# Kernel tuning notes

Hardware: AMD Instinct MI355X
Metric: run time of the kernel (lower is better)

The kernel has to match this reference:

```python
import jax, jax.numpy as jnp
import numpy as np

B, S, C, D = 2, 2048, 2048, 128
H = C // D
EPS = 1.1920928955078125e-07  # torch finfo(float32).eps (RMSNorm default eps=None)


def rms_norm(x, g):
    # x: [..., D], normalized over last dim, elementwise affine g
    var = jnp.mean(jnp.square(x), axis=-1, keepdims=True)
    return x * jax.lax.rsqrt(var + EPS) * g


def apply_rotary(x, rope):
    # x: [B,S,H,D]; rope: [S,1,D/2,2,2] (2x2 rotation matrices)
    b, s, h, d = x.shape
    x_ = x.reshape(b, s, h, d // 2, 1, 2)
    out = jnp.sum(rope * x_, axis=-1)  # [B,S,H,D/2,2]
    return out.reshape(b, s, h, d)


def setup_inputs() -> dict:
    key = jax.random.key(0)
    ks = jax.random.split(key, 10)
    sc = 1.0 / np.sqrt(C)
    return {
        "x": jax.random.normal(ks[0], (B, S, C), jnp.float32),
        "rope": jax.random.normal(ks[1], (S, 1, D // 2, 2, 2), jnp.float32),
        "Wq": jax.random.normal(ks[2], (C, C), jnp.float32) * sc,
        "bq": jnp.zeros((C,), jnp.float32),
        "Wk": jax.random.normal(ks[3], (C, C), jnp.float32) * sc,
        "bk": jnp.zeros((C,), jnp.float32),
        "Wv": jax.random.normal(ks[4], (C, C), jnp.float32) * sc,
        "bv": jnp.zeros((C,), jnp.float32),
        "gq": jnp.ones((D,), jnp.float32),
        "gk": jnp.ones((D,), jnp.float32),
        "Wo": jax.random.normal(ks[5], (C, C), jnp.float32) * sc,
        "bo": jnp.zeros((C,), jnp.float32),
    }


def reference(x, rope, Wq, bq, Wk, bk, Wv, bv, gq, gk, Wo, bo):
    b, s, _ = x.shape
    # QKV projections (torch Linear: x @ W.T + b)
    q = (x @ Wq.T + bq).reshape(b, s, H, D)
    k = (x @ Wk.T + bk).reshape(b, s, H, D)
    v = (x @ Wv.T + bv).reshape(b, s, H, D)
    # per-head RMSNorm on q/k (computed in fp32 as in the original)
    q = rms_norm(q, gq)
    k = rms_norm(k, gk)
    # rotary embedding via 2x2 rotation matrices
    q = apply_rotary(q, rope)
    k = apply_rotary(k, rope)
    # scaled dot-product attention (non-causal)
    scale = 1.0 / jnp.sqrt(jnp.asarray(D, q.dtype))
    scores = jnp.einsum("bqhd,bkhd->bhqk", q, k) * scale
    attn = jax.nn.softmax(scores, axis=-1)
    out = jnp.einsum("bhqk,bkhd->bqhd", attn, v).reshape(b, s, C)
    return out @ Wo.T + bo
```

## Files before the change

kernel.cpp:

```cpp
#include <hip/hip_runtime.h>
#include <hip/hip_bf16.h>


typedef __bf16 bf16_t;
typedef __bf16 bf16x2 __attribute__((ext_vector_type(2)));
typedef __bf16 bf16x4 __attribute__((ext_vector_type(4)));
typedef __bf16 bf16x8 __attribute__((ext_vector_type(8)));
typedef float  f32x4  __attribute__((ext_vector_type(4)));

#define EPSF 1.1920928955078125e-07f
#define QSCALE 0.1275310039f

__device__ __forceinline__ void load_lds16(const void* g, void* l) {
  __builtin_amdgcn_global_load_lds((__attribute__((address_space(1))) void*)(g),
                                   (__attribute__((address_space(3))) void*)(l),
                                   16, 0, 0);
}

__global__ __launch_bounds__(256) void castk(const float4* __restrict__ src,
                                             bf16x4* __restrict__ dst, int n4) {
  int i = blockIdx.x * blockDim.x + threadIdx.x;
  int stride = gridDim.x * blockDim.x;
  for (; i < n4; i += stride) {
    float4 v = src[i];
    bf16x4 o;
    o.x = (bf16_t)v.x; o.y = (bf16_t)v.y; o.z = (bf16_t)v.z; o.w = (bf16_t)v.w;
    dst[i] = o;
  }
}

template <int MODE>
__global__ __launch_bounds__(256, 2)
void gemm_bt(const bf16_t* __restrict__ A, const bf16_t* __restrict__ B,
             int M, int N, int K,
             const float* __restrict__ bias0, const float* __restrict__ bias1,
             const float* __restrict__ bias2,
             float* __restrict__ outf,
             bf16_t* __restrict__ qb, bf16_t* __restrict__ kb, bf16_t* __restrict__ vb) {
  __shared__ bf16_t As[128 * 64];
  __shared__ bf16_t Bs[128 * 64];
  const int t = threadIdx.x, l = t & 63, w = t >> 6;
  const int lq = l & 15, grp = l >> 4;

  int flat = blockIdx.y * gridDim.x + blockIdx.x;
  int nwg = gridDim.x * gridDim.y;
  int cpx = nwg >> 3;
  int wg = (flat & 7) * cpx + (flat >> 3);
  int bx = wg % gridDim.x, by = wg / gridDim.x;
  const int bRow = by * 128, bCol = bx * 128;
  const int wr = w >> 1, wc = w & 1;

  const int srow = w * 8 + (l >> 3);
  const int scol = ((l & 7) ^ (l >> 3)) * 8;
  const bf16_t* Ag = A + (size_t)(bRow + srow) * K + scol;
  const bf16_t* Bg = B + (size_t)(bCol + srow) * K + scol;
  const int dstbase = w * 1024;

  f32x4 acc[4][4];
  const f32x4 zf = {0.f, 0.f, 0.f, 0.f};
#pragma unroll
  for (int i = 0; i < 4; ++i)
#pragma unroll
    for (int j = 0; j < 4; ++j) acc[i][j] = zf;

  const int arow = wr * 64 + lq;
  const int brow = wc * 64 + lq;
  const int axor = l & 7;

  for (int k0 = 0; k0 < K; k0 += 64) {
#pragma unroll
    for (int c = 0; c < 4; ++c)
      load_lds16(Ag + (size_t)c * 32 * K, (char*)As + c * 4096 + dstbase);
#pragma unroll
    for (int c = 0; c < 4; ++c)
      load_lds16(Bg + (size_t)c * 32 * K, (char*)Bs + c * 4096 + dstbase);
    Ag += 64; Bg += 64;
    __syncthreads();
#pragma unroll
    for (int kk = 0; kk < 2; ++kk) {
      bf16x8 af[4], bfv[4];
#pragma unroll
      for (int i = 0; i < 4; ++i)
        af[i] = *(const bf16x8*)((const char*)As + (arow + i * 16) * 128 +
                                 (((kk << 2) + grp) ^ axor) * 16);
#pragma unroll
      for (int j = 0; j < 4; ++j)
        bfv[j] = *(const bf16x8*)((const char*)Bs + (brow + j * 16) * 128 +
                                  (((kk << 2) + grp) ^ axor) * 16);
#pragma unroll
      for (int i = 0; i < 4; ++i)
#pragma unroll
        for (int j = 0; j < 4; ++j)
          acc[i][j] = __builtin_amdgcn_mfma_f32_16x16x32_bf16(af[i], bfv[j], acc[i][j], 0, 0, 0);
    }
    __syncthreads();
  }

  if (MODE == 0) {
    const int part = bCol >> 11;
    const int hd_base = bCol & 2047;
    const int h = hd_base >> 7;
    const float* bias = part == 0 ? bias0 : part == 1 ? bias1 : bias2;
    bf16_t* dst = part == 0 ? qb : part == 1 ? kb : vb;
#pragma unroll
    for (int i = 0; i < 4; ++i)
#pragma unroll
      for (int j = 0; j < 4; ++j)
#pragma unroll
        for (int r = 0; r < 4; ++r) {
          int m = bRow + wr * 64 + i * 16 + grp * 4 + r;
          int d = wc * 64 + j * 16 + lq;
          int bb = m >> 11, s = m & 2047;
          float v = acc[i][j][r] + bias[hd_base + d];
          dst[(((size_t)bb * 16 + h) * 2048 + s) * 128 + d] = (bf16_t)v;
        }
  } else {
#pragma unroll
    for (int i = 0; i < 4; ++i)
#pragma unroll
      for (int j = 0; j < 4; ++j)
#pragma unroll
        for (int r = 0; r < 4; ++r) {
          int m = bRow + wr * 64 + i * 16 + grp * 4 + r;
          int n = bCol + wc * 64 + j * 16 + lq;
          outf[(size_t)m * N + n] = acc[i][j][r] + bias0[n];
        }
  }
}

__global__ __launch_bounds__(256)
void normrope(bf16_t* __restrict__ q, bf16_t* __restrict__ k,
              const float* __restrict__ rope,
              const float* __restrict__ gq, const float* __restrict__ gk) {
  const int l = threadIdx.x & 63, wv = threadIdx.x >> 6;
  const int rid = blockIdx.x * 4 + wv;
  const int s = rid & 2047;
  const size_t base = (size_t)rid * 128 + 2 * l;
  const float4 rp = *(const float4*)(rope + ((size_t)s * 64 + l) * 4);
  const float g0q = gq[2 * l], g1q = gq[2 * l + 1];
  const float g0k = gk[2 * l], g1k = gk[2 * l + 1];

  {
    bf16x2 xq = *(const bf16x2*)(q + base);
    float x0 = (float)xq.x, x1 = (float)xq.y;
    float ss = x0 * x0 + x1 * x1;
#pragma unroll
    for (int off = 1; off < 64; off <<= 1) ss += __shfl_xor(ss, off);
    float rs = rsqrtf(ss * (1.f / 128.f) + EPSF);
    float n0 = x0 * rs * g0q, n1 = x1 * rs * g1q;
    bf16x2 o;
    o.x = (bf16_t)((rp.x * n0 + rp.y * n1) * QSCALE);
    o.y = (bf16_t)((rp.z * n0 + rp.w * n1) * QSCALE);
    *(bf16x2*)(q + base) = o;
  }
  {
    bf16x2 xk = *(const bf16x2*)(k + base);
    float x0 = (float)xk.x, x1 = (float)xk.y;
    float ss = x0 * x0 + x1 * x1;
#pragma unroll
    for (int off = 1; off < 64; off <<= 1) ss += __shfl_xor(ss, off);
    float rs = rsqrtf(ss * (1.f / 128.f) + EPSF);
    float n0 = x0 * rs * g0k, n1 = x1 * rs * g1k;
    bf16x2 o;
    o.x = (bf16_t)(rp.x * n0 + rp.y * n1);
    o.y = (bf16_t)(rp.z * n0 + rp.w * n1);
    *(bf16x2*)(k + base) = o;
  }
}

__global__ __launch_bounds__(256)
void transpose_v(const bf16_t* __restrict__ v, bf16_t* __restrict__ vt) {
  __shared__ bf16_t st[64][68];
  const int t = threadIdx.x;
  const int bh = blockIdx.z;
  const int s0 = blockIdx.x * 64, d0 = blockIdx.y * 64;
  const bf16_t* vp = v + (size_t)bh * 2048 * 128;
  bf16_t* vtp = vt + (size_t)bh * 128 * 2048;
  const int r = t >> 4, c = (t & 15) * 4;
#pragma unroll
  for (int p = 0; p < 4; ++p) {
    bf16x4 x = *(const bf16x4*)(vp + (size_t)(s0 + r + p * 16) * 128 + d0 + c);
    *(bf16x4*)&st[r + p * 16][c] = x;
  }
  __syncthreads();
#pragma unroll
  for (int p = 0; p < 4; ++p) {
    int dr = r + p * 16;
    bf16x4 y;
    y.x = st[c + 0][dr]; y.y = st[c + 1][dr]; y.z = st[c + 2][dr]; y.w = st[c + 3][dr];
    *(bf16x4*)(vtp + (size_t)(d0 + dr) * 2048 + s0 + c) = y;
  }
}

__global__ __launch_bounds__(256, 2)
void attn_fwd(const bf16_t* __restrict__ Q, const bf16_t* __restrict__ K,
              const bf16_t* __restrict__ VT, bf16_t* __restrict__ O) {
  __shared__ char smem[81920];
  const int t = threadIdx.x, l = t & 63, wv = t >> 6;
  const int lq = l & 15, grp = l >> 4;
  const int bid = blockIdx.x;
  const int xcd = bid & 7, ksid = bid >> 3;
  const int bh = ((ksid >> 4) << 3) | xcd;
  const int qbi = ksid & 15;
  const int b_ = bh >> 4, h = bh & 15;
  const bf16_t* Qp = Q + (size_t)bh * 2048 * 128;
  const bf16_t* Kp = K + (size_t)bh * 2048 * 128;
  const bf16_t* Vp = VT + (size_t)bh * 128 * 2048;
  const int q0 = qbi * 128 + wv * 32;
  const int axor = lq & 7;

  int ksoff[4], vsoff[4], dstoff[4];
#pragma unroll
  for (int i = 0; i < 4; ++i) {
    int g = (i * 4 + wv) * 64 + l;
    int kr = g >> 4, kc = g & 15;
    ksoff[i] = kr * 256 + ((kc ^ (kr & 7)) << 4);
    int vr = g >> 3, vc = g & 7;
    vsoff[i] = vr * 4096 + ((vc ^ (vr & 7)) << 4);
    dstoff[i] = (i * 4 + wv) * 1024;
  }

  bf16x8 qf[2][4];
#pragma unroll
  for (int qt = 0; qt < 2; ++qt)
#pragma unroll
    for (int c = 0; c < 4; ++c)
      qf[qt][c] = *(const bf16x8*)(Qp + (size_t)(q0 + qt * 16 + lq) * 128 + c * 32 + grp * 8);

  f32x4 o[2][8];
  const f32x4 zf = {0.f, 0.f, 0.f, 0.f};
#pragma unroll
  for (int a = 0; a < 2; ++a)
#pragma unroll
    for (int d = 0; d < 8; ++d) o[a][d] = zf;
  float m_run[2] = {-1e30f, -1e30f}, l_run[2] = {0.f, 0.f};
  char* pb = smem + 65536 + wv * 4096;

  auto stage = [&](int buf, int kvb) {
    char* kdst = smem + buf * 16384;
    char* vdst = smem + 32768 + buf * 16384;
    const char* ksrc = (const char*)Kp + (size_t)kvb * 256;
    const char* vsrc = (const char*)Vp + (size_t)kvb * 2;
#pragma unroll
    for (int i = 0; i < 4; ++i) load_lds16(ksrc + ksoff[i], kdst + dstoff[i]);
#pragma unroll
    for (int i = 0; i < 4; ++i) load_lds16(vsrc + vsoff[i], vdst + dstoff[i]);
  };

  stage(0, 0);
  __syncthreads();

  for (int it = 0; it < 32; ++it) {
    const int cur = it & 1;
    if (it < 31) stage(cur ^ 1, (it + 1) * 64);
    const char* kb = smem + cur * 16384;
    const char* vb = smem + 32768 + cur * 16384;

    f32x4 sc[4][2];
#pragma unroll
    for (int kvt = 0; kvt < 4; ++kvt) { sc[kvt][0] = zf; sc[kvt][1] = zf; }
    __builtin_amdgcn_s_setprio(1);
#pragma unroll
    for (int kvt = 0; kvt < 4; ++kvt)
#pragma unroll
      for (int c = 0; c < 4; ++c) {
        bf16x8 kf = *(const bf16x8*)(kb + (kvt * 16 + lq) * 256 +
                                     ((((c << 2) + grp) ^ axor) << 4));
        sc[kvt][0] = __builtin_amdgcn_mfma_f32_16x16x32_bf16(kf, qf[0][c], sc[kvt][0], 0, 0, 0);
        sc[kvt][1] = __builtin_amdgcn_mfma_f32_16x16x32_bf16(kf, qf[1][c], sc[kvt][1], 0, 0, 0);
      }
    __builtin_amdgcn_s_setprio(0);

#pragma unroll
    for (int qt = 0; qt < 2; ++qt) {
      float tm = sc[0][qt][0];
#pragma unroll
      for (int kvt = 0; kvt < 4; ++kvt)
#pragma unroll
        for (int r = 0; r < 4; ++r) tm = fmaxf(tm, sc[kvt][qt][r]);
      tm = fmaxf(tm, __shfl_xor(tm, 16));
      tm = fmaxf(tm, __shfl_xor(tm, 32));
      float mnew = fmaxf(m_run[qt], tm);
      float ts = 0.f;
      const int prow = (qt * 16 + lq) * 128;
#pragma unroll
      for (int kvt = 0; kvt < 4; ++kvt) {
        float p0 = exp2f(sc[kvt][qt][0] - mnew);
        float p1 = exp2f(sc[kvt][qt][1] - mnew);
        float p2 = exp2f(sc[kvt][qt][2] - mnew);
        float p3 = exp2f(sc[kvt][qt][3] - mnew);
        ts += (p0 + p1) + (p2 + p3);
        bf16x4 w;
        w.x = (bf16_t)p0; w.y = (bf16_t)p1; w.z = (bf16_t)p2; w.w = (bf16_t)p3;
        *(bf16x4*)(pb + prow + ((((kvt << 1) | (grp >> 1)) ^ axor) << 4) +
                   ((grp & 1) << 3)) = w;
      }
      ts += __shfl_xor(ts, 16);
      ts += __shfl_xor(ts, 32);
      float alpha = exp2f(m_run[qt] - mnew);
      m_run[qt] = mnew;
      l_run[qt] = l_run[qt] * alpha + ts;
      float ar0 = __shfl(alpha, (l & 48) | (grp * 4 + 0));
      float ar1 = __shfl(alpha, (l & 48) | (grp * 4 + 1));
      float ar2 = __shfl(alpha, (l & 48) | (grp * 4 + 2));
      float ar3 = __shfl(alpha, (l & 48) | (grp * 4 + 3));
#pragma unroll
      for (int dc = 0; dc < 8; ++dc) {
        o[qt][dc][0] *= ar0; o[qt][dc][1] *= ar1;
        o[qt][dc][2] *= ar2; o[qt][dc][3] *= ar3;
      }
    }

    bf16x8 pa[2][2];
#pragma unroll
    for (int qt = 0; qt < 2; ++qt)
#pragma unroll
      for (int ks = 0; ks < 2; ++ks)
        pa[qt][ks] = *(const bf16x8*)(pb + (qt * 16 + lq) * 128 +
                                      ((((ks << 2) | grp) ^ axor) << 4));
    __builtin_amdgcn_s_setprio(1);
#pragma unroll
    for (int dc = 0; dc < 8; ++dc)
#pragma unroll
      for (int ks = 0; ks < 2; ++ks) {
        bf16x8 vf = *(const bf16x8*)(vb + (dc * 16 + lq) * 128 +
                                     ((((ks << 2) + grp) ^ axor) << 4));
        o[0][dc] = __builtin_amdgcn_mfma_f32_16x16x32_bf16(pa[0][ks], vf, o[0][dc], 0, 0, 0);
        o[1][dc] = __builtin_amdgcn_mfma_f32_16x16x32_bf16(pa[1][ks], vf, o[1][dc], 0, 0, 0);
      }
    __builtin_amdgcn_s_setprio(0);
    __syncthreads();
  }

#pragma unroll
  for (int qt = 0; qt < 2; ++qt) {
    float i0 = 1.f / __shfl(l_run[qt], (l & 48) | (grp * 4 + 0));
    float i1 = 1.f / __shfl(l_run[qt], (l & 48) | (grp * 4 + 1));
    float i2 = 1.f / __shfl(l_run[qt], (l & 48) | (grp * 4 + 2));
    float i3 = 1.f / __shfl(l_run[qt], (l & 48) | (grp * 4 + 3));
#pragma unroll
    for (int dc = 0; dc < 8; ++dc) {
      int d = dc * 16 + lq;
      int sg = q0 + qt * 16 + grp * 4;
      O[(((size_t)b_ * 2048 + sg + 0) * 16 + h) * 128 + d] = (bf16_t)(o[qt][dc][0] * i0);
      O[(((size_t)b_ * 2048 + sg + 1) * 16 + h) * 128 + d] = (bf16_t)(o[qt][dc][1] * i1);
      O[(((size_t)b_ * 2048 + sg + 2) * 16 + h) * 128 + d] = (bf16_t)(o[qt][dc][2] * i2);
      O[(((size_t)b_ * 2048 + sg + 3) * 16 + h) * 128 + d] = (bf16_t)(o[qt][dc][3] * i3);
    }
  }
}

extern "C" void kernel_launch(void* const* d_in, const int* in_sizes, int n_in,
                              void* d_out, int out_size, void* d_ws, size_t ws_size,
                              hipStream_t stream) {
  const float* x    = (const float*)d_in[0];
  const float* rope = (const float*)d_in[1];
  const float* Wq   = (const float*)d_in[2];
  const float* bq   = (const float*)d_in[3];
  const float* Wk   = (const float*)d_in[4];
  const float* bk   = (const float*)d_in[5];
  const float* Wv   = (const float*)d_in[6];
  const float* bv   = (const float*)d_in[7];
  const float* gq   = (const float*)d_in[8];
  const float* gk   = (const float*)d_in[9];
  const float* Wo   = (const float*)d_in[10];
  const float* bo   = (const float*)d_in[11];
  float* out = (float*)d_out;
  char* ws = (char*)d_ws;

  bf16_t* xbf  = (bf16_t*)(ws);
  bf16_t* wqkv = (bf16_t*)(ws + 16777216);
  bf16_t* wobf = (bf16_t*)(ws + 41943040);
  bf16_t* qb   = (bf16_t*)(ws + 50331648);
  bf16_t* kb   = (bf16_t*)(ws + 67108864);
  bf16_t* vb   = (bf16_t*)(ws + 83886080);
  bf16_t* vtb  = (bf16_t*)(ws);
  bf16_t* aob  = (bf16_t*)(ws + 16777216);

  castk<<<2048, 256, 0, stream>>>((const float4*)x, (bf16x4*)xbf, 8388608 / 4);
  castk<<<1024, 256, 0, stream>>>((const float4*)Wq, (bf16x4*)wqkv, 4194304 / 4);
  castk<<<1024, 256, 0, stream>>>((const float4*)Wk, (bf16x4*)(wqkv + 4194304), 4194304 / 4);
  castk<<<1024, 256, 0, stream>>>((const float4*)Wv, (bf16x4*)(wqkv + 8388608), 4194304 / 4);
  castk<<<1024, 256, 0, stream>>>((const float4*)Wo, (bf16x4*)wobf, 4194304 / 4);

  gemm_bt<0><<<dim3(48, 32), 256, 0, stream>>>(xbf, wqkv, 4096, 6144, 2048,
                                               bq, bk, bv, nullptr, qb, kb, vb);
  normrope<<<16384, 256, 0, stream>>>(qb, kb, rope, gq, gk);
  transpose_v<<<dim3(32, 2, 32), 256, 0, stream>>>(vb, vtb);
  attn_fwd<<<512, 256, 0, stream>>>(qb, kb, vtb, aob);
  gemm_bt<1><<<dim3(16, 32), 256, 0, stream>>>(aob, wobf, 4096, 2048, 2048,
                                               bo, nullptr, nullptr, out,
                                               nullptr, nullptr, nullptr);
}
```

Before: 451.7 us.

## Merge cast kernels and restructure attention into 8 waves with register-resident P

The five fp32-to-bf16 cast launches become one cast_all kernel. Attention now runs 512 threads per block, with each wave owning 16 query rows instead of 32, which halves per-wave register state. The P tile no longer round-trips through LDS; it stays in registers using packed bf16 conversion and permlane swap instructions to form the MFMA operand. The kernel also uses a lazy rescale that only updates the running max when it grows by more than 8, and switches to the native exp2 builtin. The trade-off is more waves contending for the same staged K/V tiles, plus inline-asm permlane ops that only exist on newer CDNA targets.

```diff
diff --git a/kernel.cpp b/kernel.cpp
--- a/kernel.cpp
+++ b/kernel.cpp
@@ -17,15 +17,28 @@
                                    16, 0, 0);
 }
 
-__global__ __launch_bounds__(256) void castk(const float4* __restrict__ src,
-                                             bf16x4* __restrict__ dst, int n4) {
+__global__ __launch_bounds__(256)
+void cast_all(const float4* __restrict__ x, const float4* __restrict__ wq,
+              const float4* __restrict__ wk, const float4* __restrict__ wv,
+              const float4* __restrict__ wo,
+              bf16x4* __restrict__ xd, bf16x4* __restrict__ wqkvd,
+              bf16x4* __restrict__ wod) {
   int i = blockIdx.x * blockDim.x + threadIdx.x;
   int stride = gridDim.x * blockDim.x;
-  for (; i < n4; i += stride) {
-    float4 v = src[i];
+  for (; i < 6291456; i += stride) {
+    float4 v;
+    bf16x4* dst;
+    if (i < 2097152) {
+      v = x[i]; dst = xd + i;
+    } else {
+      int j = i - 2097152;
+      int part = j >> 20, off = j & 1048575;
+      v = (part == 0 ? wq : part == 1 ? wk : part == 2 ? wv : wo)[off];
+      dst = part < 3 ? (wqkvd + (part << 20) + off) : (wod + off);
+    }
     bf16x4 o;
     o.x = (bf16_t)v.x; o.y = (bf16_t)v.y; o.z = (bf16_t)v.z; o.w = (bf16_t)v.w;
-    dst[i] = o;
+    *dst = o;
   }
 }
 
@@ -192,10 +205,10 @@
   }
 }
 
-__global__ __launch_bounds__(256, 2)
+__global__ __launch_bounds__(512, 4)
 void attn_fwd(const bf16_t* __restrict__ Q, const bf16_t* __restrict__ K,
               const bf16_t* __restrict__ VT, bf16_t* __restrict__ O) {
-  __shared__ char smem[81920];
+  __shared__ __align__(16) char smem[65536];
   const int t = threadIdx.x, l = t & 63, wv = t >> 6;
   const int lq = l & 15, grp = l >> 4;
   const int bid = blockIdx.x;
@@ -206,35 +219,30 @@
   const bf16_t* Qp = Q + (size_t)bh * 2048 * 128;
   const bf16_t* Kp = K + (size_t)bh * 2048 * 128;
   const bf16_t* Vp = VT + (size_t)bh * 128 * 2048;
-  const int q0 = qbi * 128 + wv * 32;
+  const int q0 = qbi * 128 + wv * 16;
   const int axor = lq & 7;
 
-  int ksoff[4], vsoff[4], dstoff[4];
-#pragma unroll
-  for (int i = 0; i < 4; ++i) {
-    int g = (i * 4 + wv) * 64 + l;
+  int ksoff[2], vsoff[2], dstoff[2];
+#pragma unroll
+  for (int i = 0; i < 2; ++i) {
+    int g = i * 512 + t;
     int kr = g >> 4, kc = g & 15;
     ksoff[i] = kr * 256 + ((kc ^ (kr & 7)) << 4);
     int vr = g >> 3, vc = g & 7;
     vsoff[i] = vr * 4096 + ((vc ^ (vr & 7)) << 4);
-    dstoff[i] = (i * 4 + wv) * 1024;
-  }
-
-  bf16x8 qf[2][4];
-#pragma unroll
-  for (int qt = 0; qt < 2; ++qt)
-#pragma unroll
-    for (int c = 0; c < 4; ++c)
-      qf[qt][c] = *(const bf16x8*)(Qp + (size_t)(q0 + qt * 16 + lq) * 128 + c * 32 + grp * 8);
-
-  f32x4 o[2][8];
+    dstoff[i] = i * 8192 + wv * 1024;
+  }
+
+  bf16x8 qf[4];
+#pragma unroll
+  for (int c = 0; c < 4; ++c)
+    qf[c] = *(const bf16x8*)(Qp + (size_t)(q0 + lq) * 128 + c * 32 + grp * 8);
+
+  f32x4 o[8];
   const f32x4 zf = {0.f, 0.f, 0.f, 0.f};
 #pragma unroll
-  for (int a = 0; a < 2; ++a)
-#pragma unroll
-    for (int d = 0; d < 8; ++d) o[a][d] = zf;
-  float m_run[2] = {-1e30f, -1e30f}, l_run[2] = {0.f, 0.f};
-  char* pb = smem + 65536 + wv * 4096;
+  for (int d = 0; d < 8; ++d) o[d] = zf;
+  float m_run = -1e30f, l_run = 0.f;
 
   auto stage = [&](int buf, int kvb) {
     char* kdst = smem + buf * 16384;
@@ -242,9 +250,9 @@
     const char* ksrc = (const char*)Kp + (size_t)kvb * 256;
     const char* vsrc = (const char*)Vp + (size_t)kvb * 2;
 #pragma unroll
-    for (int i = 0; i < 4; ++i) load_lds16(ksrc + ksoff[i], kdst + dstoff[i]);
-#pragma unroll
-    for (int i = 0; i < 4; ++i) load_lds16(vsrc + vsoff[i], vdst + dstoff[i]);
+    for (int i = 0; i < 2; ++i) load_lds16(ksrc + ksoff[i], kdst + dstoff[i]);
+#pragma unroll
+    for (int i = 0; i < 2; ++i) load_lds16(vsrc + vsoff[i], vdst + dstoff[i]);
   };
 
   stage(0, 0);
@@ -256,9 +264,9 @@
     const char* kb = smem + cur * 16384;
     const char* vb = smem + 32768 + cur * 16384;
 
-    f32x4 sc[4][2];
-#pragma unroll
-    for (int kvt = 0; kvt < 4; ++kvt) { sc[kvt][0] = zf; sc[kvt][1] = zf; }
+    f32x4 sc[4];
+#pragma unroll
+    for (int kvt = 0; kvt < 4; ++kvt) sc[kvt] = zf;
     __builtin_amdgcn_s_setprio(1);
 #pragma unroll
     for (int kvt = 0; kvt < 4; ++kvt)
@@ -266,58 +274,62 @@
       for (int c = 0; c < 4; ++c) {
         bf16x8 kf = *(const bf16x8*)(kb + (kvt * 16 + lq) * 256 +
                                      ((((c << 2) + grp) ^ axor) << 4));
-        sc[kvt][0] = __builtin_amdgcn_mfma_f32_16x16x32_bf16(kf, qf[0][c], sc[kvt][0], 0, 0, 0);
-        sc[kvt][1] = __builtin_amdgcn_mfma_f32_16x16x32_bf16(kf, qf[1][c], sc[kvt][1], 0, 0, 0);
+        sc[kvt] = __builtin_amdgcn_mfma_f32_16x16x32_bf16(kf, qf[c], sc[kvt], 0, 0, 0);
       }
     __builtin_amdgcn_s_setprio(0);
 
-#pragma unroll
-    for (int qt = 0; qt < 2; ++qt) {
-      float tm = sc[0][qt][0];
-#pragma unroll
-      for (int kvt = 0; kvt < 4; ++kvt)
-#pragma unroll
-        for (int r = 0; r < 4; ++r) tm = fmaxf(tm, sc[kvt][qt][r]);
-      tm = fmaxf(tm, __shfl_xor(tm, 16));
-      tm = fmaxf(tm, __shfl_xor(tm, 32));
-      float mnew = fmaxf(m_run[qt], tm);
-      float ts = 0.f;
-      const int prow = (qt * 16 + lq) * 128;
-#pragma unroll
-      for (int kvt = 0; kvt < 4; ++kvt) {
-        float p0 = exp2f(sc[kvt][qt][0] - mnew);
-        float p1 = exp2f(sc[kvt][qt][1] - mnew);
-        float p2 = exp2f(sc[kvt][qt][2] - mnew);
-        float p3 = exp2f(sc[kvt][qt][3] - mnew);
-        ts += (p0 + p1) + (p2 + p3);
-        bf16x4 w;
-        w.x = (bf16_t)p0; w.y = (bf16_t)p1; w.z = (bf16_t)p2; w.w = (bf16_t)p3;
-        *(bf16x4*)(pb + prow + ((((kvt << 1) | (grp >> 1)) ^ axor) << 4) +
-                   ((grp & 1) << 3)) = w;
-      }
-      ts += __shfl_xor(ts, 16);
-      ts += __shfl_xor(ts, 32);
-      float alpha = exp2f(m_run[qt] - mnew);
-      m_run[qt] = mnew;
-      l_run[qt] = l_run[qt] * alpha + ts;
+    float tm = fmaxf(fmaxf(fmaxf(fmaxf(sc[0][0], sc[0][1]), fmaxf(sc[0][2], sc[0][3])),
+                           fmaxf(fmaxf(sc[1][0], sc[1][1]), fmaxf(sc[1][2], sc[1][3]))),
+                     fmaxf(fmaxf(fmaxf(sc[2][0], sc[2][1]), fmaxf(sc[2][2], sc[2][3])),
+                           fmaxf(fmaxf(sc[3][0], sc[3][1]), fmaxf(sc[3][2], sc[3][3]))));
+    tm = fmaxf(tm, __shfl_xor(tm, 16));
+    tm = fmaxf(tm, __shfl_xor(tm, 32));
+    if (!__all(tm <= m_run + 8.0f)) {
+      float mnew = fmaxf(m_run, tm);
+      float alpha = __builtin_amdgcn_exp2f(m_run - mnew);
+      m_run = mnew;
+      l_run *= alpha;
       float ar0 = __shfl(alpha, (l & 48) | (grp * 4 + 0));
       float ar1 = __shfl(alpha, (l & 48) | (grp * 4 + 1));
       float ar2 = __shfl(alpha, (l & 48) | (grp * 4 + 2));
       float ar3 = __shfl(alpha, (l & 48) | (grp * 4 + 3));
 #pragma unroll
       for (int dc = 0; dc < 8; ++dc) {
-        o[qt][dc][0] *= ar0; o[qt][dc][1] *= ar1;
-        o[qt][dc][2] *= ar2; o[qt][dc][3] *= ar3;
+        o[dc][0] *= ar0; o[dc][1] *= ar1;
+        o[dc][2] *= ar2; o[dc][3] *= ar3;
       }
     }
-
-    bf16x8 pa[2][2];
-#pragma unroll
-    for (int qt = 0; qt < 2; ++qt)
-#pragma unroll
-      for (int ks = 0; ks < 2; ++ks)
-        pa[qt][ks] = *(const bf16x8*)(pb + (qt * 16 + lq) * 128 +
-                                      ((((ks << 2) | grp) ^ axor) << 4));
+    float p[4][4];
+    float ts = 0.f;
+#pragma unroll
+    for (int kvt = 0; kvt < 4; ++kvt) {
+      p[kvt][0] = __builtin_amdgcn_exp2f(sc[kvt][0] - m_run);
+      p[kvt][1] = __builtin_amdgcn_exp2f(sc[kvt][1] - m_run);
+      p[kvt][2] = __builtin_amdgcn_exp2f(sc[kvt][2] - m_run);
+      p[kvt][3] = __builtin_amdgcn_exp2f(sc[kvt][3] - m_run);
+      ts += (p[kvt][0] + p[kvt][1]) + (p[kvt][2] + p[kvt][3]);
+    }
+    ts += __shfl_xor(ts, 16);
+    ts += __shfl_xor(ts, 32);
+    l_run += ts;
+
+    unsigned w_[4][2];
+#pragma unroll
+    for (int kvt = 0; kvt < 4; ++kvt) {
+      asm("v_cvt_pk_bf16_f32 %0, %1, %2" : "=v"(w_[kvt][0]) : "v"(p[kvt][0]), "v"(p[kvt][1]));
+      asm("v_cvt_pk_bf16_f32 %0, %1, %2" : "=v"(w_[kvt][1]) : "v"(p[kvt][2]), "v"(p[kvt][3]));
+    }
+    union { unsigned u[4]; bf16x8 v; } pa[2];
+#pragma unroll
+    for (int ks = 0; ks < 2; ++ks)
+#pragma unroll
+      for (int hh = 0; hh < 2; ++hh) {
+        unsigned a = w_[2 * ks][hh], b = w_[2 * ks + 1][hh];
+        asm volatile("v_permlane32_swap_b32 %0, %1" : "+v"(a), "+v"(b));
+        asm volatile("v_permlane16_swap_b32 %0, %1" : "+v"(a), "+v"(b));
+        pa[ks].u[hh] = a; pa[ks].u[2 + hh] = b;
+      }
+
     __builtin_amdgcn_s_setprio(1);
 #pragma unroll
     for (int dc = 0; dc < 8; ++dc)
@@ -325,28 +337,24 @@
       for (int ks = 0; ks < 2; ++ks) {
         bf16x8 vf = *(const bf16x8*)(vb + (dc * 16 + lq) * 128 +
                                      ((((ks << 2) + grp) ^ axor) << 4));
-        o[0][dc] = __builtin_amdgcn_mfma_f32_16x16x32_bf16(pa[0][ks], vf, o[0][dc], 0, 0, 0);
-        o[1][dc] = __builtin_amdgcn_mfma_f32_16x16x32_bf16(pa[1][ks], vf, o[1][dc], 0, 0, 0);
+        o[dc] = __builtin_amdgcn_mfma_f32_16x16x32_bf16(pa[ks].v, vf, o[dc], 0, 0, 0);
       }
     __builtin_amdgcn_s_setprio(0);
     __syncthreads();
   }
 
-#pragma unroll
-  for (int qt = 0; qt < 2; ++qt) {
-    float i0 = 1.f / __shfl(l_run[qt], (l & 48) | (grp * 4 + 0));
-    float i1 = 1.f / __shfl(l_run[qt], (l & 48) | (grp * 4 + 1));
-    float i2 = 1.f / __shfl(l_run[qt], (l & 48) | (grp * 4 + 2));
-    float i3 = 1.f / __shfl(l_run[qt], (l & 48) | (grp * 4 + 3));
-#pragma unroll
-    for (int dc = 0; dc < 8; ++dc) {
-      int d = dc * 16 + lq;
-      int sg = q0 + qt * 16 + grp * 4;
-      O[(((size_t)b_ * 2048 + sg + 0) * 16 + h) * 128 + d] = (bf16_t)(o[qt][dc][0] * i0);
-      O[(((size_t)b_ * 2048 + sg + 1) * 16 + h) * 128 + d] = (bf16_t)(o[qt][dc][1] * i1);
-      O[(((size_t)b_ * 2048 + sg + 2) * 16 + h) * 128 + d] = (bf16_t)(o[qt][dc][2] * i2);
-      O[(((size_t)b_ * 2048 + sg + 3) * 16 + h) * 128 + d] = (bf16_t)(o[qt][dc][3] * i3);
-    }
+  float i0 = 1.f / __shfl(l_run, (l & 48) | (grp * 4 + 0));
+  float i1 = 1.f / __shfl(l_run, (l & 48) | (grp * 4 + 1));
+  float i2 = 1.f / __shfl(l_run, (l & 48) | (grp * 4 + 2));
+  float i3 = 1.f / __shfl(l_run, (l & 48) | (grp * 4 + 3));
+#pragma unroll
+  for (int dc = 0; dc < 8; ++dc) {
+    int d = dc * 16 + lq;
+    int sg = q0 + grp * 4;
+    O[(((size_t)b_ * 2048 + sg + 0) * 16 + h) * 128 + d] = (bf16_t)(o[dc][0] * i0);
+    O[(((size_t)b_ * 2048 + sg + 1) * 16 + h) * 128 + d] = (bf16_t)(o[dc][1] * i1);
+    O[(((size_t)b_ * 2048 + sg + 2) * 16 + h) * 128 + d] = (bf16_t)(o[dc][2] * i2);
+    O[(((size_t)b_ * 2048 + sg + 3) * 16 + h) * 128 + d] = (bf16_t)(o[dc][3] * i3);
   }
 }
 
@@ -377,17 +385,16 @@
   bf16_t* vtb  = (bf16_t*)(ws);
   bf16_t* aob  = (bf16_t*)(ws + 16777216);
 
-  castk<<<2048, 256, 0, stream>>>((const float4*)x, (bf16x4*)xbf, 8388608 / 4);
-  castk<<<1024, 256, 0, stream>>>((const float4*)Wq, (bf16x4*)wqkv, 4194304 / 4);
-  castk<<<1024, 256, 0, stream>>>((const float4*)Wk, (bf16x4*)(wqkv + 4194304), 4194304 / 4);
-  castk<<<1024, 256, 0, stream>>>((const float4*)Wv, (bf16x4*)(wqkv + 8388608), 4194304 / 4);
-  castk<<<1024, 256, 0, stream>>>((const float4*)Wo, (bf16x4*)wobf, 4194304 / 4);
+  cast_all<<<2048, 256, 0, stream>>>((const float4*)x, (const float4*)Wq,
+                                     (const float4*)Wk, (const float4*)Wv,
+                                     (const float4*)Wo,
+                                     (bf16x4*)xbf, (bf16x4*)wqkv, (bf16x4*)wobf);
 
   gemm_bt<0><<<dim3(48, 32), 256, 0, stream>>>(xbf, wqkv, 4096, 6144, 2048,
                                                bq, bk, bv, nullptr, qb, kb, vb);
   normrope<<<16384, 256, 0, stream>>>(qb, kb, rope, gq, gk);
   transpose_v<<<dim3(32, 2, 32), 256, 0, stream>>>(vb, vtb);
-  attn_fwd<<<512, 256, 0, stream>>>(qb, kb, vtb, aob);
+  attn_fwd<<<512, 512, 0, stream>>>(qb, kb, vtb, aob);
   gemm_bt<1><<<dim3(16, 32), 256, 0, stream>>>(aob, wobf, 4096, 2048, 2048,
                                                bo, nullptr, nullptr, out,
                                                nullptr, nullptr, nullptr);
```

After: 424.2 us. 6.1% less time.
